# Kernel optimization log

Hardware: AMD Instinct MI355X
Metric: run time of the kernel (lower is better)

Reference implementation:

```python
import jax, jax.numpy as jnp
import numpy as np

B = 32768  # batch of intersections (original code is batch=1)
# phase pair construction from the original forward:
# phase_demand[k] = demand[a_k] + demand[b_k]
PAIRS_A = np.array([0, 0, 4, 1, 2, 2, 6, 3])
PAIRS_B = np.array([4, 1, 5, 5, 6, 3, 7, 7])


def _competition_mask():
    m = np.ones((8, 8), np.float32)
    np.fill_diagonal(m, 0.0)
    for i, j in [(0, 1), (0, 2), (1, 3), (2, 3), (4, 5), (4, 6), (5, 7), (6, 7)]:
        m[i, j] = 0.5
        m[j, i] = 0.5
    return jnp.asarray(m)


def setup_inputs() -> dict:
    key = jax.random.key(0)
    ks = jax.random.split(key, 16)
    n = lambda k, shape: jax.random.normal(k, shape, dtype=jnp.float32) * 0.3
    inp = {
        'x': jax.random.normal(ks[0], (B, 16), dtype=jnp.float32),
        'mask': _competition_mask(),
        # demand_model_vehicle: Linear(1,2) ReLU Linear(2,4) ReLU
        'wv1': n(ks[1], (1, 2)), 'bv1': jnp.zeros((2,), jnp.float32),
        'wv2': n(ks[2], (2, 4)), 'bv2': jnp.zeros((4,), jnp.float32),
        # demand_model_phase: Linear(1,2) ReLU Linear(2,4) ReLU
        'wp1': n(ks[3], (1, 2)), 'bp1': jnp.zeros((2,), jnp.float32),
        'wp2': n(ks[4], (2, 4)), 'bp2': jnp.zeros((4,), jnp.float32),
        # embedding: Linear(8,16) ReLU
        'we': n(ks[5], (8, 16)), 'be': jnp.zeros((16,), jnp.float32),
        # conv_pair: 1x1 convs 32->20->20 with ReLU
        'wc1': n(ks[6], (32, 20)), 'bc1': jnp.zeros((20,), jnp.float32),
        'wc2': n(ks[7], (20, 20)), 'bc2': jnp.zeros((20,), jnp.float32),
        # conv_mask_pair: 1x1 convs 1->4->20->20 with ReLU
        'wm1': n(ks[8], (1, 4)), 'bm1': jnp.zeros((4,), jnp.float32),
        'wm2': n(ks[9], (4, 20)), 'bm2': jnp.zeros((20,), jnp.float32),
        'wm3': n(ks[10], (20, 20)), 'bm3': jnp.zeros((20,), jnp.float32),
        # conv_competition: 1x1 convs 20->8->1 (no ReLU)
        'wk1': n(ks[11], (20, 8)), 'bk1': jnp.zeros((8,), jnp.float32),
        'wk2': n(ks[12], (8, 1)), 'bk2': jnp.zeros((1,), jnp.float32),
    }
    return inp


def reference(x, mask, wv1, bv1, wv2, bv2, wp1, bp1, wp2, bp2, we, be,
              wc1, bc1, wc2, bc2, wm1, bm1, wm2, bm2, wm3, bm3,
              wk1, bk1, wk2, bk2):
    b = x.shape[0]
    veh = x[:, :8, None]   # [B,8,1] vehicle counts (fed to demand_model_vehicle)
    pha = x[:, 8:, None]   # [B,8,1] phase bits (fed to demand_model_phase)
    dv = jax.nn.relu(jax.nn.relu(veh @ wv1 + bv1) @ wv2 + bv2)  # [B,8,4]
    dp = jax.nn.relu(jax.nn.relu(pha @ wp1 + bp1) @ wp2 + bp2)  # [B,8,4]
    demand = jax.nn.relu(jnp.concatenate([dv, dp], -1) @ we + be)  # [B,8,16]
    # phase-pair demands
    pd = demand[:, PAIRS_A] + demand[:, PAIRS_B]  # [B,8,16]
    # pairwise concat: pair[i,j] = cat(pd[i], pd[j])  -> [B,8,8,32]
    pair = jnp.concatenate([
        jnp.broadcast_to(pd[:, :, None, :], (b, 8, 8, 16)),
        jnp.broadcast_to(pd[:, None, :, :], (b, 8, 8, 16)),
    ], -1)
    # conv_pair (1x1 convs == channel-dim linears)
    h = jax.nn.relu(pair @ wc1 + bc1)
    h = jax.nn.relu(h @ wc2 + bc2)            # [B,8,8,20]
    # conv_mask_pair on the fixed competition mask
    y = jax.nn.relu(mask[..., None] @ wm1 + bm1)
    y = jax.nn.relu(y @ wm2 + bm2)
    y = jax.nn.relu(y @ wm3 + bm3)            # [8,8,20]
    r = h * y                                  # masked messages [B,8,8,20]
    z = (r @ wk1 + bk1) @ wk2 + bk2            # [B,8,8,1]
    return jnp.sum(z, axis=-1)                 # sum over channel dim -> [B,8,8]
```

## Files before the change

kernel.cpp:

```cpp
#include <hip/hip_runtime.h>

#define BLK 256
#define NW 4
#define GRID 2048

typedef float f32x2 __attribute__((ext_vector_type(2)));

__device__ __forceinline__ float relu_(float v) { return fmaxf(v, 0.f); }
__device__ __forceinline__ void wave_sync() {
    asm volatile("s_waitcnt lgkmcnt(0)" ::: "memory");
}

#define PA_PACK 0x36221400u
#define PB_PACK 0x77365514u

__global__ void yk_kernel(
    const float* __restrict__ mask,
    const float* __restrict__ wm1, const float* __restrict__ bm1,
    const float* __restrict__ wm2, const float* __restrict__ bm2,
    const float* __restrict__ wm3, const float* __restrict__ bm3,
    const float* __restrict__ wk1, const float* __restrict__ bk1,
    const float* __restrict__ wk2, const float* __restrict__ bk2,
    float* __restrict__ ws)
{
    int tid = threadIdx.x;
    int ij = tid >> 2, coff = (tid & 3) * 5;
    int i = ij >> 3, j = ij & 7;
    float m = mask[i * 8 + j];
    float a[4];
#pragma unroll
    for (int q = 0; q < 4; q++) a[q] = relu_(fmaf(m, wm1[q], bm1[q]));
    float b2[20];
#pragma unroll
    for (int c = 0; c < 20; c++) {
        float acc = bm2[c];
#pragma unroll
        for (int q = 0; q < 4; q++) acc = fmaf(a[q], wm2[q * 20 + c], acc);
        b2[c] = relu_(acc);
    }
#pragma unroll
    for (int cc = 0; cc < 5; cc++) {
        int c = coff + cc;
        float acc = bm3[c];
#pragma unroll
        for (int k = 0; k < 20; k++) acc = fmaf(b2[k], wm3[k * 20 + c], acc);
        float y = relu_(acc);
        float wkk = 0.f;
#pragma unroll
        for (int q = 0; q < 8; q++) wkk = fmaf(wk1[c * 8 + q], wk2[q], wkk);
        ws[ij * 20 + c] = y * wkk;
    }
    if (tid == 0) {
        float c0 = bk2[0];
#pragma unroll
        for (int q = 0; q < 8; q++) c0 = fmaf(bk1[q], wk2[q], c0);
        ws[1280] = c0;
    }
}

__global__ __launch_bounds__(BLK, 6) void frap_kernel(
    const float* __restrict__ x,
    const float* __restrict__ wv1, const float* __restrict__ bv1,
    const float* __restrict__ wv2, const float* __restrict__ bv2,
    const float* __restrict__ wp1, const float* __restrict__ bp1,
    const float* __restrict__ wp2, const float* __restrict__ bp2,
    const float* __restrict__ we,  const float* __restrict__ be,
    const float* __restrict__ wc1, const float* __restrict__ bc1,
    const float* __restrict__ wc2, const float* __restrict__ bc2,
    const float* __restrict__ ykg,
    float* __restrict__ out, int Btot)
{
    __shared__ float s_sw[32];
    __shared__ float s_wet[16][12];
    __shared__ float s_wc1t[20][36];
    __shared__ float s_bc1[20];
    __shared__ float s_be[16];
    __shared__ float s_cat[NW][8][8];
    __shared__ float s_pd[NW][8][20];
    __shared__ float s_u[NW][8][20];
    __shared__ float s_v[NW][8][20];

    const int tid  = threadIdx.x;
    const int w    = tid >> 6;
    const int lane = tid & 63;

    if (tid < 32) {
        int base = tid & 15, grp = tid >> 4;
        const float* W1 = grp ? wp1 : wv1;
        const float* B1 = grp ? bp1 : bv1;
        const float* W2 = grp ? wp2 : wv2;
        const float* B2 = grp ? bp2 : bv2;
        float v;
        if      (base < 2)  v = W1[base];
        else if (base < 4)  v = B1[base - 2];
        else if (base < 12) v = W2[base - 4];
        else                v = B2[base - 12];
        s_sw[tid] = v;
    }
    if (tid < 128) s_wet[tid & 15][tid >> 4] = we[tid];
    for (int idx = tid; idx < 640; idx += BLK) {
        int k = idx / 20, c = idx - k * 20;
        s_wc1t[c][k] = wc1[idx];
    }
    if (tid < 20) s_bc1[tid] = bc1[tid];
    if (tid < 16) s_be[tid]  = be[tid];
    __syncthreads();

    float yk[20];
#pragma unroll
    for (int c = 0; c < 20; c++) yk[c] = ykg[lane * 20 + c];
    const float c0 = ykg[1280];

    const int i4 = lane >> 3, j4 = lane & 7;

    for (int b0 = blockIdx.x * NW; b0 < Btot; b0 += gridDim.x * NW) {
        const int b = b0 + w;

        {
            int e = lane >> 3, f = lane & 7;
            int sb = (f >= 4) ? 16 : 0;
            int q  = f & 3;
            float s  = x[b * 16 + ((f >= 4) ? 8 + e : e)];
            float t0 = relu_(fmaf(s, s_sw[sb + 0], s_sw[sb + 2]));
            float t1 = relu_(fmaf(s, s_sw[sb + 1], s_sw[sb + 3]));
            s_cat[w][e][f] = relu_(fmaf(t0, s_sw[sb + 4 + q],
                                  fmaf(t1, s_sw[sb + 8 + q], s_sw[sb + 12 + q])));
        }
        wave_sync();

#pragma unroll
        for (int r = 0; r < 2; r++) {
            int idx = lane + 64 * r;
            int i = idx >> 4, k = idx & 15;
            int pa = (PA_PACK >> (4 * i)) & 15;
            int pb = (PB_PACK >> (4 * i)) & 15;
            const float* ca = &s_cat[w][pa][0];
            const float* cb = &s_cat[w][pb][0];
            const float* wf = &s_wet[k][0];
            float da = s_be[k], db = da;
#pragma unroll
            for (int f = 0; f < 8; f++) {
                float wv = wf[f];
                da = fmaf(ca[f], wv, da);
                db = fmaf(cb[f], wv, db);
            }
            s_pd[w][i][k] = relu_(da) + relu_(db);
        }
        wave_sync();

        {
            int row = lane >> 2, cg = lane & 3;
            int uv = row >> 3, i = row & 7;
            const int coff = cg * 5;
            float pdr[16];
#pragma unroll
            for (int k = 0; k < 16; k++) pdr[k] = s_pd[w][i][k];
            float acc[5];
#pragma unroll
            for (int cc = 0; cc < 5; cc++) acc[cc] = uv ? 0.f : s_bc1[coff + cc];
#pragma unroll
            for (int cc = 0; cc < 5; cc++) {
                const float* wr = &s_wc1t[coff + cc][uv * 16];
#pragma unroll
                for (int k = 0; k < 16; k++)
                    acc[cc] = fmaf(pdr[k], wr[k], acc[cc]);
            }
            float* dst = uv ? &s_v[w][i][0] : &s_u[w][i][0];
#pragma unroll
            for (int cc = 0; cc < 5; cc++) dst[coff + cc] = acc[cc];
        }
        wave_sync();

        {
            float h1[20];
#pragma unroll
            for (int k = 0; k < 20; k++)
                h1[k] = relu_(s_u[w][i4][k] + s_v[w][j4][k]);

            f32x2 s2[10];
#pragma unroll
            for (int c = 0; c < 10; c++) {
                s2[c].x = bc2[2 * c];
                s2[c].y = bc2[2 * c + 1];
            }
#pragma unroll
            for (int k = 0; k < 20; k++) {
                f32x2 hk; hk.x = h1[k]; hk.y = h1[k];
                const f32x2* wr = (const f32x2*)&wc2[k * 20];
#pragma unroll
                for (int c = 0; c < 10; c++)
                    s2[c] += hk * wr[c];
            }
            float z = c0;
#pragma unroll
            for (int c = 0; c < 10; c++) {
                z = fmaf(relu_(s2[c].x), yk[2 * c],     z);
                z = fmaf(relu_(s2[c].y), yk[2 * c + 1], z);
            }
            out[b * 64 + lane] = z;
        }
    }
}

extern "C" void kernel_launch(void* const* d_in, const int* in_sizes, int n_in,
                              void* d_out, int out_size, void* d_ws, size_t ws_size,
                              hipStream_t stream) {
    const float* x    = (const float*)d_in[0];
    const float* mask = (const float*)d_in[1];
    const float* wv1  = (const float*)d_in[2];
    const float* bv1  = (const float*)d_in[3];
    const float* wv2  = (const float*)d_in[4];
    const float* bv2  = (const float*)d_in[5];
    const float* wp1  = (const float*)d_in[6];
    const float* bp1  = (const float*)d_in[7];
    const float* wp2  = (const float*)d_in[8];
    const float* bp2  = (const float*)d_in[9];
    const float* we   = (const float*)d_in[10];
    const float* be   = (const float*)d_in[11];
    const float* wc1  = (const float*)d_in[12];
    const float* bc1  = (const float*)d_in[13];
    const float* wc2  = (const float*)d_in[14];
    const float* bc2  = (const float*)d_in[15];
    const float* wm1  = (const float*)d_in[16];
    const float* bm1  = (const float*)d_in[17];
    const float* wm2  = (const float*)d_in[18];
    const float* bm2  = (const float*)d_in[19];
    const float* wm3  = (const float*)d_in[20];
    const float* bm3  = (const float*)d_in[21];
    const float* wk1  = (const float*)d_in[22];
    const float* bk1  = (const float*)d_in[23];
    const float* wk2  = (const float*)d_in[24];
    const float* bk2  = (const float*)d_in[25];
    float* out = (float*)d_out;
    float* ws  = (float*)d_ws;

    int Btot = in_sizes[0] / 16;

    yk_kernel<<<1, 256, 0, stream>>>(mask, wm1, bm1, wm2, bm2, wm3, bm3,
                                     wk1, bk1, wk2, bk2, ws);

    int grid = Btot / NW;
    if (grid > GRID) grid = GRID;

    frap_kernel<<<grid, BLK, 0, stream>>>(
        x, wv1, bv1, wv2, bv2, wp1, bp1, wp2, bp2, we, be,
        wc1, bc1, wc2, bc2, ws, out, Btot);
}
```

Baseline: 43.03 us.

## Compute full conv_pair first layer per lane instead of factored u/v precompute

Removes the factored u+v decomposition of the first 1x1 conv (a per-row precompute staged through shared memory) and has each lane compute the full 32->20 layer for its (i,j) pair directly, with packed f32x2 FMAs and weights read from global memory. This drops one shared-memory staging stage and a wave sync, but raises the per-lane FMA count from roughly 20 adds to 320 FMAs. Launch bounds occupancy is lowered from 6 to 4 to allow more registers.

```diff
diff --git a/kernel.cpp b/kernel.cpp
--- a/kernel.cpp
+++ b/kernel.cpp
@@ -5,6 +5,7 @@
 #define GRID 2048
 
 typedef float f32x2 __attribute__((ext_vector_type(2)));
+typedef float f32x4 __attribute__((ext_vector_type(4)));
 
 __device__ __forceinline__ float relu_(float v) { return fmaxf(v, 0.f); }
 __device__ __forceinline__ void wave_sync() {
@@ -58,7 +59,7 @@
     }
 }
 
-__global__ __launch_bounds__(BLK, 6) void frap_kernel(
+__global__ __launch_bounds__(BLK, 4) void frap_kernel(
     const float* __restrict__ x,
     const float* __restrict__ wv1, const float* __restrict__ bv1,
     const float* __restrict__ wv2, const float* __restrict__ bv2,
@@ -72,13 +73,9 @@
 {
     __shared__ float s_sw[32];
     __shared__ float s_wet[16][12];
-    __shared__ float s_wc1t[20][36];
-    __shared__ float s_bc1[20];
     __shared__ float s_be[16];
     __shared__ float s_cat[NW][8][8];
     __shared__ float s_pd[NW][8][20];
-    __shared__ float s_u[NW][8][20];
-    __shared__ float s_v[NW][8][20];
 
     const int tid  = threadIdx.x;
     const int w    = tid >> 6;
@@ -98,12 +95,7 @@
         s_sw[tid] = v;
     }
     if (tid < 128) s_wet[tid & 15][tid >> 4] = we[tid];
-    for (int idx = tid; idx < 640; idx += BLK) {
-        int k = idx / 20, c = idx - k * 20;
-        s_wc1t[c][k] = wc1[idx];
-    }
-    if (tid < 20) s_bc1[tid] = bc1[tid];
-    if (tid < 16) s_be[tid]  = be[tid];
+    if (tid < 16)  s_be[tid] = be[tid];
     __syncthreads();
 
     float yk[20];
@@ -149,33 +141,38 @@
         wave_sync();
 
         {
-            int row = lane >> 2, cg = lane & 3;
-            int uv = row >> 3, i = row & 7;
-            const int coff = cg * 5;
-            float pdr[16];
-#pragma unroll
-            for (int k = 0; k < 16; k++) pdr[k] = s_pd[w][i][k];
-            float acc[5];
-#pragma unroll
-            for (int cc = 0; cc < 5; cc++) acc[cc] = uv ? 0.f : s_bc1[coff + cc];
-#pragma unroll
-            for (int cc = 0; cc < 5; cc++) {
-                const float* wr = &s_wc1t[coff + cc][uv * 16];
-#pragma unroll
-                for (int k = 0; k < 16; k++)
-                    acc[cc] = fmaf(pdr[k], wr[k], acc[cc]);
-            }
-            float* dst = uv ? &s_v[w][i][0] : &s_u[w][i][0];
-#pragma unroll
-            for (int cc = 0; cc < 5; cc++) dst[coff + cc] = acc[cc];
-        }
-        wave_sync();
-
-        {
-            float h1[20];
-#pragma unroll
-            for (int k = 0; k < 20; k++)
-                h1[k] = relu_(s_u[w][i4][k] + s_v[w][j4][k]);
+            float pdi[16], pdj[16];
+#pragma unroll
+            for (int k = 0; k < 16; k += 4) {
+                *(f32x4*)&pdi[k] = *(const f32x4*)&s_pd[w][i4][k];
+                *(f32x4*)&pdj[k] = *(const f32x4*)&s_pd[w][j4][k];
+            }
+
+            f32x2 h[10];
+#pragma unroll
+            for (int c = 0; c < 10; c++) {
+                h[c].x = bc1[2 * c];
+                h[c].y = bc1[2 * c + 1];
+            }
+#pragma unroll
+            for (int k = 0; k < 16; k++) {
+                f32x2 pk_; pk_.x = pdi[k]; pk_.y = pdi[k];
+                const f32x2* wr = (const f32x2*)&wc1[k * 20];
+#pragma unroll
+                for (int c = 0; c < 10; c++) h[c] += pk_ * wr[c];
+            }
+#pragma unroll
+            for (int k = 0; k < 16; k++) {
+                f32x2 pk_; pk_.x = pdj[k]; pk_.y = pdj[k];
+                const f32x2* wr = (const f32x2*)&wc1[(16 + k) * 20];
+#pragma unroll
+                for (int c = 0; c < 10; c++) h[c] += pk_ * wr[c];
+            }
+#pragma unroll
+            for (int c = 0; c < 10; c++) {
+                h[c].x = relu_(h[c].x);
+                h[c].y = relu_(h[c].y);
+            }
 
             f32x2 s2[10];
 #pragma unroll
@@ -185,12 +182,13 @@
             }
 #pragma unroll
             for (int k = 0; k < 20; k++) {
-                f32x2 hk; hk.x = h1[k]; hk.y = h1[k];
+                float hk = (k & 1) ? h[k >> 1].y : h[k >> 1].x;
+                f32x2 hv; hv.x = hk; hv.y = hk;
                 const f32x2* wr = (const f32x2*)&wc2[k * 20];
 #pragma unroll
-                for (int c = 0; c < 10; c++)
-                    s2[c] += hk * wr[c];
-            }
+                for (int c = 0; c < 10; c++) s2[c] += hv * wr[c];
+            }
+
             float z = c0;
 #pragma unroll
             for (int c = 0; c < 10; c++) {
```

After: 69.83 us. +62.3%, slower.

## Hoist per-lane weights into registers and vectorize LDS reads with packed FMAs

Applied to the files above, without the earlier changes.

Loop-invariant per-lane values (demand-MLP weights, pair indices, bias, and the 80 wc1 weights for this lane's stage-3 slice) are loaded once before the batch loop instead of being re-read from shared memory each iteration. Stage 2 and 3 LDS reads become 128-bit vector loads with packed f32x2 FMAs, and the yk vector is reloaded from global memory each iteration rather than held in 20 registers. The launch-bounds occupancy hint drops from 6 to 3 blocks per CU to make room for the larger register footprint. This trades lower occupancy and extra global/L1 traffic for fewer LDS instructions.

```diff
diff --git a/kernel.cpp b/kernel.cpp
--- a/kernel.cpp
+++ b/kernel.cpp
@@ -5,6 +5,7 @@
 #define GRID 2048
 
 typedef float f32x2 __attribute__((ext_vector_type(2)));
+typedef float f32x4 __attribute__((ext_vector_type(4)));
 
 __device__ __forceinline__ float relu_(float v) { return fmaxf(v, 0.f); }
 __device__ __forceinline__ void wave_sync() {
@@ -58,7 +59,7 @@
     }
 }
 
-__global__ __launch_bounds__(BLK, 6) void frap_kernel(
+__global__ __launch_bounds__(BLK, 3) void frap_kernel(
     const float* __restrict__ x,
     const float* __restrict__ wv1, const float* __restrict__ bv1,
     const float* __restrict__ wv2, const float* __restrict__ bv2,
@@ -106,76 +107,103 @@
     if (tid < 16) s_be[tid]  = be[tid];
     __syncthreads();
 
-    float yk[20];
-#pragma unroll
-    for (int c = 0; c < 20; c++) yk[c] = ykg[lane * 20 + c];
+    const int e1 = lane >> 3, f1 = lane & 7;
+    const int sb = (f1 >= 4) ? 16 : 0, q1 = f1 & 3;
+    const float sw0 = s_sw[sb + 0], sw1 = s_sw[sb + 1];
+    const float sw2 = s_sw[sb + 2], sw3 = s_sw[sb + 3];
+    const float sw4 = s_sw[sb + 4 + q1], sw8 = s_sw[sb + 8 + q1],
+                sw12 = s_sw[sb + 12 + q1];
+    const int x_off = (f1 >= 4) ? 8 + e1 : e1;
+
+    const int k2 = lane & 15;
+    const float beK = s_be[k2];
+    const int i2a = lane >> 4;
+    const int paA = (PA_PACK >> (4 * i2a)) & 15;
+    const int pbA = (PB_PACK >> (4 * i2a)) & 15;
+    const int paB = (PA_PACK >> (4 * (i2a + 4))) & 15;
+    const int pbB = (PB_PACK >> (4 * (i2a + 4))) & 15;
+
+    const int row3 = lane >> 2, cg3 = lane & 3;
+    const int uv3 = row3 >> 3, i3 = row3 & 7, coff3 = cg3 * 5;
+    float bc1r[5];
+#pragma unroll
+    for (int cc = 0; cc < 5; cc++) bc1r[cc] = uv3 ? 0.f : s_bc1[coff3 + cc];
+    f32x2 wreg[40];
+#pragma unroll
+    for (int kk = 0; kk < 8; kk++)
+#pragma unroll
+        for (int cc = 0; cc < 5; cc++)
+            wreg[kk * 5 + cc] = *(const f32x2*)&s_wc1t[coff3 + cc][uv3 * 16 + 2 * kk];
+    float* const dst3 = (uv3 ? &s_v[w][i3][0] : &s_u[w][i3][0]) + coff3;
+
+    const int i4 = lane >> 3, j4 = lane & 7;
     const float c0 = ykg[1280];
-
-    const int i4 = lane >> 3, j4 = lane & 7;
+    const float* const ykp = ykg + lane * 20;
 
     for (int b0 = blockIdx.x * NW; b0 < Btot; b0 += gridDim.x * NW) {
         const int b = b0 + w;
 
         {
-            int e = lane >> 3, f = lane & 7;
-            int sb = (f >= 4) ? 16 : 0;
-            int q  = f & 3;
-            float s  = x[b * 16 + ((f >= 4) ? 8 + e : e)];
-            float t0 = relu_(fmaf(s, s_sw[sb + 0], s_sw[sb + 2]));
-            float t1 = relu_(fmaf(s, s_sw[sb + 1], s_sw[sb + 3]));
-            s_cat[w][e][f] = relu_(fmaf(t0, s_sw[sb + 4 + q],
-                                  fmaf(t1, s_sw[sb + 8 + q], s_sw[sb + 12 + q])));
+            float s  = x[b * 16 + x_off];
+            float t0 = relu_(fmaf(s, sw0, sw2));
+            float t1 = relu_(fmaf(s, sw1, sw3));
+            s_cat[w][e1][f1] = relu_(fmaf(t0, sw4, fmaf(t1, sw8, sw12)));
         }
         wave_sync();
 
-#pragma unroll
-        for (int r = 0; r < 2; r++) {
-            int idx = lane + 64 * r;
-            int i = idx >> 4, k = idx & 15;
-            int pa = (PA_PACK >> (4 * i)) & 15;
-            int pb = (PB_PACK >> (4 * i)) & 15;
-            const float* ca = &s_cat[w][pa][0];
-            const float* cb = &s_cat[w][pb][0];
-            const float* wf = &s_wet[k][0];
-            float da = s_be[k], db = da;
-#pragma unroll
-            for (int f = 0; f < 8; f++) {
-                float wv = wf[f];
-                da = fmaf(ca[f], wv, da);
-                db = fmaf(cb[f], wv, db);
-            }
-            s_pd[w][i][k] = relu_(da) + relu_(db);
+        {
+            union { f32x4 v4[2]; f32x2 v2[4]; } wfu;
+            wfu.v4[0] = *(const f32x4*)&s_wet[k2][0];
+            wfu.v4[1] = *(const f32x4*)&s_wet[k2][4];
+#pragma unroll
+            for (int r = 0; r < 2; r++) {
+                const int pa = r ? paB : paA;
+                const int pb = r ? pbB : pbA;
+                union { f32x4 v4[2]; f32x2 v2[4]; } ca, cb;
+                ca.v4[0] = *(const f32x4*)&s_cat[w][pa][0];
+                ca.v4[1] = *(const f32x4*)&s_cat[w][pa][4];
+                cb.v4[0] = *(const f32x4*)&s_cat[w][pb][0];
+                cb.v4[1] = *(const f32x4*)&s_cat[w][pb][4];
+                f32x2 da2 = {beK, 0.f}, db2 = {beK, 0.f};
+#pragma unroll
+                for (int f = 0; f < 4; f++) {
+                    da2 += ca.v2[f] * wfu.v2[f];
+                    db2 += cb.v2[f] * wfu.v2[f];
+                }
+                s_pd[w][i2a + 4 * r][k2] = relu_(da2.x + da2.y) + relu_(db2.x + db2.y);
+            }
         }
         wave_sync();
 
         {
-            int row = lane >> 2, cg = lane & 3;
-            int uv = row >> 3, i = row & 7;
-            const int coff = cg * 5;
-            float pdr[16];
-#pragma unroll
-            for (int k = 0; k < 16; k++) pdr[k] = s_pd[w][i][k];
-            float acc[5];
-#pragma unroll
-            for (int cc = 0; cc < 5; cc++) acc[cc] = uv ? 0.f : s_bc1[coff + cc];
-#pragma unroll
-            for (int cc = 0; cc < 5; cc++) {
-                const float* wr = &s_wc1t[coff + cc][uv * 16];
-#pragma unroll
-                for (int k = 0; k < 16; k++)
-                    acc[cc] = fmaf(pdr[k], wr[k], acc[cc]);
-            }
-            float* dst = uv ? &s_v[w][i][0] : &s_u[w][i][0];
-#pragma unroll
-            for (int cc = 0; cc < 5; cc++) dst[coff + cc] = acc[cc];
+            union { f32x4 v4[4]; f32x2 v2[8]; } pdu;
+#pragma unroll
+            for (int t = 0; t < 4; t++)
+                pdu.v4[t] = *(const f32x4*)&s_pd[w][i3][4 * t];
+            f32x2 acc[5];
+#pragma unroll
+            for (int cc = 0; cc < 5; cc++) { acc[cc].x = bc1r[cc]; acc[cc].y = 0.f; }
+#pragma unroll
+            for (int kk = 0; kk < 8; kk++)
+#pragma unroll
+                for (int cc = 0; cc < 5; cc++)
+                    acc[cc] += pdu.v2[kk] * wreg[kk * 5 + cc];
+#pragma unroll
+            for (int cc = 0; cc < 5; cc++)
+                dst3[cc] = acc[cc].x + acc[cc].y;
         }
         wave_sync();
 
         {
+            union { f32x4 v4[5]; f32x2 v2[10]; float f[20]; } ur, vr;
+#pragma unroll
+            for (int t = 0; t < 5; t++) {
+                ur.v4[t] = *(const f32x4*)&s_u[w][i4][4 * t];
+                vr.v4[t] = *(const f32x4*)&s_v[w][j4][4 * t];
+            }
             float h1[20];
 #pragma unroll
-            for (int k = 0; k < 20; k++)
-                h1[k] = relu_(s_u[w][i4][k] + s_v[w][j4][k]);
+            for (int k = 0; k < 20; k++) h1[k] = relu_(ur.f[k] + vr.f[k]);
 
             f32x2 s2[10];
 #pragma unroll
@@ -185,17 +213,21 @@
             }
 #pragma unroll
             for (int k = 0; k < 20; k++) {
-                f32x2 hk; hk.x = h1[k]; hk.y = h1[k];
+                f32x2 hv; hv.x = h1[k]; hv.y = h1[k];
                 const f32x2* wr = (const f32x2*)&wc2[k * 20];
 #pragma unroll
-                for (int c = 0; c < 10; c++)
-                    s2[c] += hk * wr[c];
-            }
+                for (int c = 0; c < 10; c++) s2[c] += hv * wr[c];
+            }
+
+            f32x4 yk4[5];
+#pragma unroll
+            for (int t = 0; t < 5; t++) yk4[t] = *(const f32x4*)&ykp[4 * t];
+
             float z = c0;
 #pragma unroll
             for (int c = 0; c < 10; c++) {
-                z = fmaf(relu_(s2[c].x), yk[2 * c],     z);
-                z = fmaf(relu_(s2[c].y), yk[2 * c + 1], z);
+                z = fmaf(relu_(s2[c].x), yk4[(2 * c) >> 2][(2 * c) & 3],     z);
+                z = fmaf(relu_(s2[c].y), yk4[(2 * c + 1) >> 2][(2 * c + 1) & 3], z);
             }
             out[b * 64 + lane] = z;
         }
```

Result: slower. 47.20 us (+9.7%).
